# Kernel optimization log

Measured on AMD Instinct MI355X. Metric: run time of the kernel, lower is better.

The kernel has to match this reference:

```python
import jax, jax.numpy as jnp
import numpy as np

V, R, A, C, T = 50000, 5, 8, 32, 32  # vertices, radial, angular, in-channels, templates
DELTA = 2                             # rotation_delta -> n_rotations = A // DELTA = 4


def setup_inputs() -> dict:
    key = jax.random.key(0)
    ks = jax.random.split(key, 6)
    signal = jax.random.normal(ks[0], (V, C), jnp.float32)
    bc_idx = jax.random.randint(ks[1], (V, R, A, 3), 0, V, dtype=jnp.int32)
    w = jax.random.uniform(ks[2], (V, R, A, 3), jnp.float32)
    bc_w = w / jnp.sum(w, axis=-1, keepdims=True)  # barycentric weights sum to 1
    templ1 = jax.random.normal(ks[3], (T, R, A, C), jnp.float32) * 0.05
    bias1 = jnp.zeros((T,), jnp.float32)
    templ2 = jax.random.normal(ks[4], (T, R, A, T), jnp.float32) * 0.05
    bias2 = jnp.zeros((T,), jnp.float32)
    return {"signal": signal, "bc_idx": bc_idx, "bc_w": bc_w,
            "templ1": templ1, "bias1": bias1, "templ2": templ2, "bias2": bias2}


def _conv_dirac(x, bc_idx, bc_w, templ, bias):
    """Dirac intrinsic surface convolution.
    x: [V, Cin]; bc_idx/bc_w: [V, R, A, 3]; templ: [T, R, A, Cin] -> [V, n_rot, T]."""
    # Barycentric interpolation of the mesh signal at template vertices.
    gathered = x[bc_idx]                                   # [V, R, A, 3, Cin]
    interp = jnp.einsum('vrai,vraic->vrac', bc_w, gathered)  # [V, R, A, Cin]
    n_rot = A // DELTA
    # Rotating the patch by +s angular steps == correlating with templ rolled by +s.
    rot_t = jnp.stack([jnp.roll(templ, r * DELTA, axis=2) for r in range(n_rot)])  # [n_rot, T, R, A, Cin]
    return jnp.einsum('vrac,ntrac->vnt', interp, rot_t) + bias  # [V, n_rot, T]


def _amp(x):
    # AngularMaxPooling: max over the rotation axis.
    return jnp.max(x, axis=1)


def reference(signal, bc_idx, bc_w, templ1, bias1, templ2, bias2):
    s = jax.nn.relu(_conv_dirac(signal, bc_idx, bc_w, templ1, bias1))  # conv1 (relu)
    s = _amp(s)                                                        # [V, T]
    s = _conv_dirac(s, bc_idx, bc_w, templ2, bias2)                    # conv2 (linear)
    s = _amp(s)                                                        # [V, T]
    # input_dim == amt_templates -> no rescale branch; residual add + output relu
    return jax.nn.relu(s + signal)
```

## Files before the change

### kernel.cpp

```cpp
#include <hip/hip_runtime.h>
#include <hip/hip_bf16.h>

#define VN 50000
#define RN 5
#define AN 8
#define CN 32
#define NB 8
#define MT 32

typedef short bf16x8  __attribute__((ext_vector_type(8)));
typedef short bf16x16 __attribute__((ext_vector_type(16)));
typedef float f32x4   __attribute__((ext_vector_type(4)));
typedef int   i32x4   __attribute__((ext_vector_type(4)));

__device__ __forceinline__ float b2f(short s) {
    union { unsigned u; float f; } cv;
    cv.u = ((unsigned)(unsigned short)s) << 16;
    return cv.f;
}
__device__ __forceinline__ short f2b(float f) {
    union { float f; unsigned u; } cv; cv.f = f;
    unsigned r = cv.u + 0x7fff + ((cv.u >> 16) & 1);
    return (short)(r >> 16);
}

__global__ void pack_x(const float* __restrict__ x, __hip_bfloat16* __restrict__ xb, int n4) {
    int i = blockIdx.x * blockDim.x + threadIdx.x;
    if (i >= n4) return;
    float4 v = ((const float4*)x)[i];
    ushort4 o;
    o.x = (unsigned short)f2b(v.x);
    o.y = (unsigned short)f2b(v.y);
    o.z = (unsigned short)f2b(v.z);
    o.w = (unsigned short)f2b(v.w);
    ((ushort4*)xb)[i] = o;
}

__global__ void build_Bp(const float* __restrict__ t1, const float* __restrict__ t2,
                         __hip_bfloat16* __restrict__ B1, __hip_bfloat16* __restrict__ B2) {
    int m = blockIdx.x * blockDim.x + threadIdx.x;
    if (m >= RN * AN * NB * 64 * 8) return;
    int j = m & 7;
    int lane = (m >> 3) & 63;
    int nb = (m >> 9) & 7;
    int kstep = m >> 12;
    int c = ((lane >> 4) << 3) + j;
    int r = kstep >> 3, a = kstep & 7;
    int nt = nb * 16 + (lane & 15);
    int n = nt >> 5, t = nt & 31;
    int asrc = (a - 2 * n + 8) & 7;
    int src = ((t * RN + r) * AN + asrc) * CN + c;
    ((unsigned short*)B1)[m] = (unsigned short)f2b(t1[src]);
    ((unsigned short*)B2)[m] = (unsigned short)f2b(t2[src]);
}

template<bool FIRST>
__global__ __launch_bounds__(128, 2)
void conv_fused(const __hip_bfloat16* __restrict__ xb,
                const int*   __restrict__ bc_idx,
                const float* __restrict__ bc_w,
                const __hip_bfloat16* __restrict__ Bp,
                const float* __restrict__ bias,
                const float* __restrict__ signal,
                __hip_bfloat16* __restrict__ out_bf,
                float* __restrict__ out_f)
{
    __shared__ __align__(16) unsigned char smraw[16384];
    const int tid = threadIdx.x;
    const int wid = tid >> 6;
    const int lane = tid & 63;
    const int vl = tid & 31;
    const int h  = (tid >> 5) & 1;
    const int vbase = blockIdx.x * MT;
    const unsigned short* xs = (const unsigned short*)xb;

    int vg = vbase + vl;
    int vc = vg < VN ? vg : VN - 1;
    const size_t ibase = (size_t)vc * 120 + wid * 12;

    const int arow = lane & 15;
    const int c0q = lane >> 4;

    f32x4 acc[2][4];
#pragma unroll
    for (int mi = 0; mi < 2; ++mi)
#pragma unroll
        for (int j = 0; j < 4; ++j) acc[mi][j] = (f32x4)(0.f);

    i32x4 I[2][3];
    f32x4 Wv[2][3];
    bf16x16 G[12];

#pragma unroll
    for (int q = 0; q < 3; ++q) {
        I[0][q]  = __builtin_nontemporal_load((const i32x4*)(bc_idx + ibase) + q);
        I[1][q]  = __builtin_nontemporal_load((const i32x4*)(bc_idx + ibase + 24) + q);
        Wv[0][q] = __builtin_nontemporal_load((const f32x4*)(bc_w  + ibase) + q);
    }
    __builtin_amdgcn_sched_barrier(0);
#pragma unroll
    for (int e = 0; e < 12; ++e) {
        int idx = I[0][e >> 2][e & 3];
        G[e] = *(const bf16x16*)(xs + (size_t)idx * CN + h * 16);
    }
    __builtin_amdgcn_sched_barrier(0);

#pragma unroll
    for (int r = 0; r < RN; ++r) {
        if (r + 2 < RN) {
#pragma unroll
            for (int q = 0; q < 3; ++q)
                I[r & 1][q] = __builtin_nontemporal_load(
                    (const i32x4*)(bc_idx + ibase + (r + 2) * 24) + q);
        }
        if (r + 1 < RN) {
#pragma unroll
            for (int q = 0; q < 3; ++q)
                Wv[(r + 1) & 1][q] = __builtin_nontemporal_load(
                    (const f32x4*)(bc_w + ibase + (r + 1) * 24) + q);
        }
        __builtin_amdgcn_sched_barrier(0);

#pragma unroll
        for (int aa = 0; aa < 4; ++aa) {
            const int a = wid * 4 + aa;
            float w0 = Wv[r & 1][(aa * 3 + 0) >> 2][(aa * 3 + 0) & 3];
            float w1 = Wv[r & 1][(aa * 3 + 1) >> 2][(aa * 3 + 1) & 3];
            float w2 = Wv[r & 1][(aa * 3 + 2) >> 2][(aa * 3 + 2) & 3];
            bf16x8 ch[2];
#pragma unroll
            for (int j = 0; j < 16; ++j) {
                float f = fmaf(w0, b2f(G[aa * 3 + 0][j]),
                         fmaf(w1, b2f(G[aa * 3 + 1][j]),
                               w2 * b2f(G[aa * 3 + 2][j])));
                ch[j >> 3][j & 7] = f2b(f);
            }
#pragma unroll
            for (int qq = 0; qq < 2; ++qq) {
                int baddr = vl * 512 + ((a * 64 + h * 32 + qq * 16) ^ ((vl & 7) << 4));
                *(bf16x8*)(smraw + baddr) = ch[qq];
            }
        }
        __syncthreads();

        if (r + 1 < RN) {
#pragma unroll
            for (int e = 0; e < 12; ++e) {
                int idx = I[(r + 1) & 1][e >> 2][e & 3];
                G[e] = *(const bf16x16*)(xs + (size_t)idx * CN + h * 16);
            }
            __builtin_amdgcn_sched_barrier(0);
        }

#pragma unroll
        for (int ks = 0; ks < 8; ++ks) {
            bf16x8 af[2];
#pragma unroll
            for (int mi = 0; mi < 2; ++mi) {
                int row = mi * 16 + arow;
                int baddr = row * 512 + ((ks * 64 + c0q * 16) ^ ((row & 7) << 4));
                af[mi] = *(const bf16x8*)(smraw + baddr);
            }
            int gks = r * 8 + ks;
#pragma unroll
            for (int j = 0; j < 4; ++j) {
                int nb = wid * 4 + j;
                bf16x8 bfr = *(const bf16x8*)((const unsigned short*)Bp +
                                ((size_t)(gks * NB + nb) * 64 + lane) * 8);
                acc[0][j] = __builtin_amdgcn_mfma_f32_16x16x32_bf16(af[0], bfr, acc[0][j], 0, 0, 0);
                acc[1][j] = __builtin_amdgcn_mfma_f32_16x16x32_bf16(af[1], bfr, acc[1][j], 0, 0, 0);
            }
        }
        __syncthreads();
    }

    f32x4* redp = (f32x4*)smraw;
#pragma unroll
    for (int mi = 0; mi < 2; ++mi)
#pragma unroll
        for (int q = 0; q < 2; ++q) {
            f32x4 pm;
#pragma unroll
            for (int rg = 0; rg < 4; ++rg)
                pm[rg] = fmaxf(acc[mi][q][rg], acc[mi][q + 2][rg]);
            redp[((wid * 2 + mi) * 2 + q) * 64 + lane] = pm;
        }
    __syncthreads();

    const int colD = lane & 15;
    const int rbase = (lane >> 4) << 2;
#pragma unroll
    for (int q = 0; q < 2; ++q) {
        f32x4 m0 = redp[((0 * 2 + wid) * 2 + q) * 64 + lane];
        f32x4 m1 = redp[((1 * 2 + wid) * 2 + q) * 64 + lane];
        int t = q * 16 + colD;
        float b = bias[t];
#pragma unroll
        for (int rg = 0; rg < 4; ++rg) {
            int vv = vbase + wid * 16 + rbase + rg;
            if (vv < VN) {
                float val = fmaxf(m0[rg], m1[rg]) + b;
                if (FIRST) {
                    ((unsigned short*)out_bf)[vv * CN + t] =
                        (unsigned short)f2b(fmaxf(val, 0.f));
                } else {
                    val += __builtin_nontemporal_load(signal + vv * CN + t);
                    __builtin_nontemporal_store(fmaxf(val, 0.f), out_f + vv * CN + t);
                }
            }
        }
    }
}

extern "C" void kernel_launch(void* const* d_in, const int* in_sizes, int n_in,
                              void* d_out, int out_size, void* d_ws, size_t ws_size,
                              hipStream_t stream) {
    const float* signal = (const float*)d_in[0];
    const int*   bc_idx = (const int*)d_in[1];
    const float* bc_w   = (const float*)d_in[2];
    const float* t1     = (const float*)d_in[3];
    const float* b1     = (const float*)d_in[4];
    const float* t2     = (const float*)d_in[5];
    const float* b2     = (const float*)d_in[6];
    float* out = (float*)d_out;

    __hip_bfloat16* ws = (__hip_bfloat16*)d_ws;
    __hip_bfloat16* xb  = ws;
    __hip_bfloat16* s1  = ws + VN * CN;
    __hip_bfloat16* Bp1 = ws + 2 * VN * CN;
    __hip_bfloat16* Bp2 = Bp1 + RN * AN * NB * 64 * 8;

    pack_x<<<(VN * CN / 4 + 255) / 256, 256, 0, stream>>>(signal, xb, VN * CN / 4);
    build_Bp<<<(RN * AN * NB * 64 * 8) / 256, 256, 0, stream>>>(t1, t2, Bp1, Bp2);

    int blocks = (VN + MT - 1) / MT;
    conv_fused<true ><<<blocks, 128, 0, stream>>>(xb, bc_idx, bc_w, Bp1, b1, nullptr, s1, nullptr);
    conv_fused<false><<<blocks, 128, 0, stream>>>(s1, bc_idx, bc_w, Bp2, b2, signal, nullptr, out);
}
```

Baseline: 228.2 us.

## Halve vertex tile to 16 per block to raise occupancy

```diff
diff --git a/kernel.cpp b/kernel.cpp
--- a/kernel.cpp
+++ b/kernel.cpp
@@ -6,12 +6,13 @@
 #define AN 8
 #define CN 32
 #define NB 8
-#define MT 32
+#define MT 16
 
 typedef short bf16x8  __attribute__((ext_vector_type(8)));
 typedef short bf16x16 __attribute__((ext_vector_type(16)));
 typedef float f32x4   __attribute__((ext_vector_type(4)));
-typedef int   i32x4   __attribute__((ext_vector_type(4)));
+typedef float f32x2   __attribute__((ext_vector_type(2)));
+typedef int   i32x2   __attribute__((ext_vector_type(2)));
 
 __device__ __forceinline__ float b2f(short s) {
     union { unsigned u; float f; } cv;
@@ -55,7 +56,7 @@
 }
 
 template<bool FIRST>
-__global__ __launch_bounds__(128, 2)
+__global__ __launch_bounds__(128, 4)
 void conv_fused(const __hip_bfloat16* __restrict__ xb,
                 const int*   __restrict__ bc_idx,
                 const float* __restrict__ bc_w,
@@ -65,42 +66,41 @@
                 __hip_bfloat16* __restrict__ out_bf,
                 float* __restrict__ out_f)
 {
-    __shared__ __align__(16) unsigned char smraw[16384];
+    __shared__ __align__(16) unsigned char smraw[8192];
     const int tid = threadIdx.x;
     const int wid = tid >> 6;
     const int lane = tid & 63;
-    const int vl = tid & 31;
-    const int h  = (tid >> 5) & 1;
+    const int vl = tid & 15;
+    const int h  = (tid >> 4) & 1;
+    const int as = tid >> 5;
     const int vbase = blockIdx.x * MT;
     const unsigned short* xs = (const unsigned short*)xb;
 
     int vg = vbase + vl;
     int vc = vg < VN ? vg : VN - 1;
-    const size_t ibase = (size_t)vc * 120 + wid * 12;
+    const size_t ibase = (size_t)vc * 120 + as * 6;
 
     const int arow = lane & 15;
     const int c0q = lane >> 4;
 
-    f32x4 acc[2][4];
-#pragma unroll
-    for (int mi = 0; mi < 2; ++mi)
-#pragma unroll
-        for (int j = 0; j < 4; ++j) acc[mi][j] = (f32x4)(0.f);
-
-    i32x4 I[2][3];
-    f32x4 Wv[2][3];
-    bf16x16 G[12];
+    f32x4 acc[4];
+#pragma unroll
+    for (int j = 0; j < 4; ++j) acc[j] = (f32x4)(0.f);
+
+    i32x2 I[2][3];
+    f32x2 Wv[2][3];
+    bf16x16 G[6];
 
 #pragma unroll
     for (int q = 0; q < 3; ++q) {
-        I[0][q]  = __builtin_nontemporal_load((const i32x4*)(bc_idx + ibase) + q);
-        I[1][q]  = __builtin_nontemporal_load((const i32x4*)(bc_idx + ibase + 24) + q);
-        Wv[0][q] = __builtin_nontemporal_load((const f32x4*)(bc_w  + ibase) + q);
+        I[0][q]  = __builtin_nontemporal_load((const i32x2*)(bc_idx + ibase) + q);
+        I[1][q]  = __builtin_nontemporal_load((const i32x2*)(bc_idx + ibase + 24) + q);
+        Wv[0][q] = __builtin_nontemporal_load((const f32x2*)(bc_w  + ibase) + q);
     }
     __builtin_amdgcn_sched_barrier(0);
 #pragma unroll
-    for (int e = 0; e < 12; ++e) {
-        int idx = I[0][e >> 2][e & 3];
+    for (int e = 0; e < 6; ++e) {
+        int idx = I[0][e >> 1][e & 1];
         G[e] = *(const bf16x16*)(xs + (size_t)idx * CN + h * 16);
     }
     __builtin_amdgcn_sched_barrier(0);
@@ -111,22 +111,22 @@
 #pragma unroll
             for (int q = 0; q < 3; ++q)
                 I[r & 1][q] = __builtin_nontemporal_load(
-                    (const i32x4*)(bc_idx + ibase + (r + 2) * 24) + q);
+                    (const i32x2*)(bc_idx + ibase + (r + 2) * 24) + q);
         }
         if (r + 1 < RN) {
 #pragma unroll
             for (int q = 0; q < 3; ++q)
                 Wv[(r + 1) & 1][q] = __builtin_nontemporal_load(
-                    (const f32x4*)(bc_w + ibase + (r + 1) * 24) + q);
+                    (const f32x2*)(bc_w + ibase + (r + 1) * 24) + q);
         }
         __builtin_amdgcn_sched_barrier(0);
 
 #pragma unroll
-        for (int aa = 0; aa < 4; ++aa) {
-            const int a = wid * 4 + aa;
-            float w0 = Wv[r & 1][(aa * 3 + 0) >> 2][(aa * 3 + 0) & 3];
-            float w1 = Wv[r & 1][(aa * 3 + 1) >> 2][(aa * 3 + 1) & 3];
-            float w2 = Wv[r & 1][(aa * 3 + 2) >> 2][(aa * 3 + 2) & 3];
+        for (int aa = 0; aa < 2; ++aa) {
+            const int a = as * 2 + aa;
+            float w0 = Wv[r & 1][(aa * 3 + 0) >> 1][(aa * 3 + 0) & 1];
+            float w1 = Wv[r & 1][(aa * 3 + 1) >> 1][(aa * 3 + 1) & 1];
+            float w2 = Wv[r & 1][(aa * 3 + 2) >> 1][(aa * 3 + 2) & 1];
             bf16x8 ch[2];
 #pragma unroll
             for (int j = 0; j < 16; ++j) {
@@ -145,8 +145,8 @@
 
         if (r + 1 < RN) {
 #pragma unroll
-            for (int e = 0; e < 12; ++e) {
-                int idx = I[(r + 1) & 1][e >> 2][e & 3];
+            for (int e = 0; e < 6; ++e) {
+                int idx = I[(r + 1) & 1][e >> 1][e & 1];
                 G[e] = *(const bf16x16*)(xs + (size_t)idx * CN + h * 16);
             }
             __builtin_amdgcn_sched_barrier(0);
@@ -154,21 +154,15 @@
 
 #pragma unroll
         for (int ks = 0; ks < 8; ++ks) {
-            bf16x8 af[2];
-#pragma unroll
-            for (int mi = 0; mi < 2; ++mi) {
-                int row = mi * 16 + arow;
-                int baddr = row * 512 + ((ks * 64 + c0q * 16) ^ ((row & 7) << 4));
-                af[mi] = *(const bf16x8*)(smraw + baddr);
-            }
+            int baddr = arow * 512 + ((ks * 64 + c0q * 16) ^ ((arow & 7) << 4));
+            bf16x8 af = *(const bf16x8*)(smraw + baddr);
             int gks = r * 8 + ks;
 #pragma unroll
             for (int j = 0; j < 4; ++j) {
                 int nb = wid * 4 + j;
                 bf16x8 bfr = *(const bf16x8*)((const unsigned short*)Bp +
                                 ((size_t)(gks * NB + nb) * 64 + lane) * 8);
-                acc[0][j] = __builtin_amdgcn_mfma_f32_16x16x32_bf16(af[0], bfr, acc[0][j], 0, 0, 0);
-                acc[1][j] = __builtin_amdgcn_mfma_f32_16x16x32_bf16(af[1], bfr, acc[1][j], 0, 0, 0);
+                acc[j] = __builtin_amdgcn_mfma_f32_16x16x32_bf16(af, bfr, acc[j], 0, 0, 0);
             }
         }
         __syncthreads();
@@ -176,28 +170,26 @@
 
     f32x4* redp = (f32x4*)smraw;
 #pragma unroll
-    for (int mi = 0; mi < 2; ++mi)
-#pragma unroll
-        for (int q = 0; q < 2; ++q) {
-            f32x4 pm;
-#pragma unroll
-            for (int rg = 0; rg < 4; ++rg)
-                pm[rg] = fmaxf(acc[mi][q][rg], acc[mi][q + 2][rg]);
-            redp[((wid * 2 + mi) * 2 + q) * 64 + lane] = pm;
-        }
+    for (int q = 0; q < 2; ++q) {
+        f32x4 pm;
+#pragma unroll
+        for (int rg = 0; rg < 4; ++rg)
+            pm[rg] = fmaxf(acc[q][rg], acc[q + 2][rg]);
+        redp[(wid * 2 + q) * 64 + lane] = pm;
+    }
     __syncthreads();
 
     const int colD = lane & 15;
     const int rbase = (lane >> 4) << 2;
-#pragma unroll
-    for (int q = 0; q < 2; ++q) {
-        f32x4 m0 = redp[((0 * 2 + wid) * 2 + q) * 64 + lane];
-        f32x4 m1 = redp[((1 * 2 + wid) * 2 + q) * 64 + lane];
+    {
+        const int q = wid;
+        f32x4 m0 = redp[(0 * 2 + q) * 64 + lane];
+        f32x4 m1 = redp[(1 * 2 + q) * 64 + lane];
         int t = q * 16 + colD;
         float b = bias[t];
 #pragma unroll
         for (int rg = 0; rg < 4; ++rg) {
-            int vv = vbase + wid * 16 + rbase + rg;
+            int vv = vbase + rbase + rg;
             if (vv < VN) {
                 float val = fmaxf(m0[rg], m1[rg]) + b;
                 if (FIRST) {
```

After: 222.3 us. 1.03x faster.
